# Performance work log

Measured on AMD Instinct MI355X. Metric: run time of the kernel, lower is better.

The kernel has to match this reference:

```python
import jax, jax.numpy as jnp
import numpy as np

S, M, H, E = 8192, 1024, 4096, 8
CAPACITY = S // E  # capacity_factor = 1.0, k = 1


def setup_inputs() -> dict:
    key = jax.random.key(0)
    ks = jax.random.split(key, 4)
    return {
        "x": jax.random.normal(ks[0], (S, M), jnp.float32),
        "wg": jax.random.normal(ks[1], (M, E), jnp.float32) * 0.02,
        "inter_w": jax.random.normal(ks[2], (E, M, H), jnp.float32) * 0.02,
        "inter_b": jnp.zeros((E, H), jnp.float32),
        "output_w": jax.random.normal(ks[3], (E, H, M), jnp.float32) * 0.02,
        "output_b": jnp.zeros((E, M), jnp.float32),
    }


def _top1_gate(x, wg, capacity):
    """GShard-style top-1 gate (inference: no noise, drop tokens over capacity).
    Returns combine_weights [S,E,C] (float) and dispatch_mask [S,E,C] (float 0/1)."""
    logits = x @ wg                                   # [S,E]
    gates = jax.nn.softmax(logits, axis=-1)           # [S,E]
    idx = jnp.argmax(gates, axis=-1)                  # [S]
    mask1 = jax.nn.one_hot(idx, gates.shape[-1], dtype=gates.dtype)  # [S,E]
    # 0-based position of each token within its expert's queue
    locations = jnp.cumsum(mask1, axis=0) - mask1     # [S,E]
    mask1 = mask1 * (locations < capacity)            # drop overflow tokens
    pos = jnp.sum(locations * mask1, axis=1).astype(jnp.int32)  # [S]
    gate_s = jnp.sum(gates * mask1, axis=1)           # [S] gate value of kept tokens
    loc_oh = jax.nn.one_hot(pos, capacity, dtype=gates.dtype)    # [S,C]
    combine = gate_s[:, None, None] * mask1[:, :, None] * loc_oh[:, None, :]  # [S,E,C]
    dispatch = (combine > 0).astype(x.dtype)
    return combine, dispatch


def reference(x, wg, inter_w, inter_b, output_w, output_b):
    combine, dispatch = _top1_gate(x, wg, CAPACITY)
    # token dispatch: torch.einsum('sec,sm->ecm', dispatch_mask, attention_output)
    disp_x = jnp.einsum('sec,sm->ecm', dispatch, x)                 # [E,C,M]
    # per-expert fused gelu-GEMM MLP (gelu_gemm_func: gelu(x@W1+b1)@W2, +b2)
    h = jax.nn.gelu(jnp.einsum('ecm,emh->ech', disp_x, inter_w)
                    + inter_b[:, None, :], approximate=False)       # [E,C,H]
    exp_out = jnp.einsum('ech,ehm->ecm', h, output_w) + output_b[:, None, :]  # [E,C,M]
    # combine: combined_weights.reshape(S, E*C) @ expert_output.reshape(E*C, M)
    y = jnp.einsum('sec,ecm->sm', combine, exp_out)                 # [S,M]
    return y
```

## Files before the change

### kernel.cpp

```cpp
#include <hip/hip_runtime.h>

#define S_ 8192
#define M_ 1024
#define H_ 4096
#define E_ 8
#define C_ 1024

typedef short s16x8 __attribute__((ext_vector_type(8)));
typedef float f32x4 __attribute__((ext_vector_type(4)));

__device__ __forceinline__ unsigned short f2bf(float f) {
    unsigned int u = __float_as_uint(f);
    unsigned int r = u + 0x7fffu + ((u >> 16) & 1u);
    return (unsigned short)(r >> 16);
}
__device__ __forceinline__ float bf2f(unsigned short s) {
    return __uint_as_float(((unsigned int)s) << 16);
}

__device__ __forceinline__ void async_copy16(const unsigned short* g, unsigned short* l) {
    __builtin_amdgcn_global_load_lds(
        (const __attribute__((address_space(1))) unsigned int*)g,
        (__attribute__((address_space(3))) unsigned int*)l, 16, 0, 0);
}

__global__ __launch_bounds__(256) void gate_kernel(
    const float* __restrict__ x, const float* __restrict__ wg,
    int* __restrict__ expert_of, float* __restrict__ gate_full,
    unsigned short* __restrict__ xb)
{
    int token = (blockIdx.x * 256 + threadIdx.x) >> 6;
    int lane  = threadIdx.x & 63;
    const float* xr = x + (size_t)token * M_;
    unsigned short* xbr = xb + (size_t)token * M_;
    double acc[E_] = {0,0,0,0,0,0,0,0};
    for (int t = 0; t < M_ / 64; ++t) {
        int m = t * 64 + lane;
        float xf = xr[m];
        xbr[m] = f2bf(xf);
        double xv = (double)xf;
        const float* w = wg + m * E_;
        #pragma unroll
        for (int e = 0; e < E_; ++e) acc[e] += xv * (double)w[e];
    }
    #pragma unroll
    for (int e = 0; e < E_; ++e)
        for (int off = 32; off; off >>= 1) acc[e] += __shfl_xor(acc[e], off);
    if (lane == 0) {
        double mx = acc[0]; int idx = 0;
        #pragma unroll
        for (int e = 1; e < E_; ++e) if (acc[e] > mx) { mx = acc[e]; idx = e; }
        double den = 0.0;
        #pragma unroll
        for (int e = 0; e < E_; ++e) den += exp(acc[e] - mx);
        expert_of[token] = idx;
        gate_full[token] = (float)(1.0 / den);
    }
}

__global__ __launch_bounds__(256) void count_kernel(
    const int* __restrict__ expert_of, int* __restrict__ cnt,
    int* __restrict__ slot_to_token)
{
    __shared__ int wc[4][E_];
    int tid = threadIdx.x, lane = tid & 63, wv = tid >> 6;
    slot_to_token[blockIdx.x * 256 + tid] = -1;
    int e = expert_of[blockIdx.x * 256 + tid];
    #pragma unroll
    for (int j = 0; j < E_; ++j) {
        unsigned long long b = __ballot(e == j);
        if (lane == 0) wc[wv][j] = __popcll(b);
    }
    __syncthreads();
    if (tid < E_) {
        int s = 0;
        #pragma unroll
        for (int w = 0; w < 4; ++w) s += wc[w][tid];
        cnt[blockIdx.x * E_ + tid] = s;
    }
}

__global__ __launch_bounds__(64) void prefix_kernel(
    const int* __restrict__ cnt, int* __restrict__ cbase)
{
    int tid = threadIdx.x;
    if (tid < E_) {
        int run = 0;
        for (int b = 0; b < 32; ++b) { cbase[b * E_ + tid] = run; run += cnt[b * E_ + tid]; }
    }
}

__global__ __launch_bounds__(256) void scatter_kernel(
    const int* __restrict__ expert_of, const int* __restrict__ cbase,
    int* __restrict__ slot_to_token)
{
    __shared__ int wc[4][E_];
    int tid = threadIdx.x, lane = tid & 63, wv = tid >> 6;
    int s = blockIdx.x * 256 + tid;
    int e = expert_of[s];
    unsigned long long mymask = 0;
    #pragma unroll
    for (int j = 0; j < E_; ++j) {
        unsigned long long b = __ballot(e == j);
        if (lane == 0) wc[wv][j] = __popcll(b);
        if (j == e) mymask = b;
    }
    __syncthreads();
    int waveoff = 0;
    for (int w = 0; w < 4; ++w) if (w < wv) waveoff += wc[w][e];
    int pos = cbase[blockIdx.x * E_ + e] + waveoff +
              __popcll(mymask & ((1ull << lane) - 1ull));
    if (pos < C_) slot_to_token[e * C_ + pos] = s;
}

__global__ __launch_bounds__(256) void transpose_cvt_kernel(
    const float* __restrict__ src, unsigned short* __restrict__ dst, int K, int N)
{
    __shared__ unsigned short tile[64 * 84];
    const size_t esz = (size_t)K * N;
    const float* s = src + (size_t)blockIdx.z * esz;
    unsigned short* d = dst + (size_t)blockIdx.z * esz;
    const int k0 = blockIdx.y * 64, n0 = blockIdx.x * 64;
    const int tid = threadIdx.x;
    {
        const int n  = tid & 63;
        const int kb = (tid >> 6) * 16;
        #pragma unroll
        for (int i = 0; i < 4; ++i) {
            int k4 = kb + i * 4;
            float a0 = s[(size_t)(k0 + k4 + 0) * N + n0 + n];
            float a1 = s[(size_t)(k0 + k4 + 1) * N + n0 + n];
            float a2 = s[(size_t)(k0 + k4 + 2) * N + n0 + n];
            float a3 = s[(size_t)(k0 + k4 + 3) * N + n0 + n];
            unsigned long long p = (unsigned long long)f2bf(a0)
                | ((unsigned long long)f2bf(a1) << 16)
                | ((unsigned long long)f2bf(a2) << 32)
                | ((unsigned long long)f2bf(a3) << 48);
            *(unsigned long long*)(&tile[n * 84 + k4]) = p;
        }
    }
    __syncthreads();
    {
        const int n  = tid >> 3;
        const int k8 = (tid & 7) * 8;
        #pragma unroll
        for (int j = 0; j < 2; ++j) {
            int nn = n + j * 32;
            unsigned long long lo = *(const unsigned long long*)(&tile[nn * 84 + k8]);
            unsigned long long hi = *(const unsigned long long*)(&tile[nn * 84 + k8 + 4]);
            ulonglong2 v; v.x = lo; v.y = hi;
            *(ulonglong2*)(d + (size_t)(n0 + nn) * K + k0 + k8) = v;
        }
    }
}


#define RD_A(BUF, I, KS) \
  (*(const s16x8*)(&AsB[BUF][(wr * 128 + (I) * 16 + ln16) * 64 + ((((KS) * 4 + qd) ^ ln7) * 8)]))
#define RD_B(BUF, J, KS) \
  (*(const s16x8*)(&BsB[BUF][(wcn * 64 + (J) * 16 + ln16) * 64 + ((((KS) * 4 + qd) ^ ln7) * 8)]))

#define STG_A(BUF, HF, KT) do { \
    async_copy16(ap[2 * (HF)]     + (size_t)(KT) * 64, dA##BUF + (2 * (HF)) * 4096); \
    async_copy16(ap[2 * (HF) + 1] + (size_t)(KT) * 64, dA##BUF + (2 * (HF) + 1) * 4096); } while (0)
#define STG_B(BUF, HF, KT) do { \
    async_copy16(bp[2 * (HF)]     + (size_t)(KT) * 64, dB##BUF + (2 * (HF)) * 4096); \
    async_copy16(bp[2 * (HF) + 1] + (size_t)(KT) * 64, dB##BUF + (2 * (HF) + 1) * 4096); } while (0)

#define MFMA16(I0, J0, BB) do { \
    __builtin_amdgcn_s_setprio(1); \
    _Pragma("unroll") \
    for (int ii = 0; ii < 4; ++ii) { \
      acc[(I0)+ii][(J0)+0] = __builtin_amdgcn_mfma_f32_16x16x32_bf16(a[ii][0], BB[0][0], acc[(I0)+ii][(J0)+0], 0, 0, 0); \
      acc[(I0)+ii][(J0)+0] = __builtin_amdgcn_mfma_f32_16x16x32_bf16(a[ii][1], BB[0][1], acc[(I0)+ii][(J0)+0], 0, 0, 0); \
      acc[(I0)+ii][(J0)+1] = __builtin_amdgcn_mfma_f32_16x16x32_bf16(a[ii][0], BB[1][0], acc[(I0)+ii][(J0)+1], 0, 0, 0); \
      acc[(I0)+ii][(J0)+1] = __builtin_amdgcn_mfma_f32_16x16x32_bf16(a[ii][1], BB[1][1], acc[(I0)+ii][(J0)+1], 0, 0, 0); \
    } \
    __builtin_amdgcn_s_setprio(0); \
} while (0)

#define BAR()  __builtin_amdgcn_s_barrier()
#define LGKM0() asm volatile("s_waitcnt lgkmcnt(0)" ::: "memory")
#define VM2()  asm volatile("s_waitcnt vmcnt(2)" ::: "memory")
#define VM0()  asm volatile("s_waitcnt vmcnt(0)" ::: "memory")

#define GEMM_8PH(NITER, NT) \
    STG_A(0, 0, 0); STG_A(0, 1, 0); STG_B(0, 0, 0); STG_B(0, 1, 0); \
    STG_A(1, 0, 1); \
    VM2(); BAR(); \
    for (int it = 0; it < (NITER); ++it) { \
        const int t1 = 2 * it + 1, t2 = 2 * it + 2, t3 = 2 * it + 3; \
         \
        _Pragma("unroll") for (int ii = 0; ii < 4; ++ii) { a[ii][0] = RD_A(0, ii, 0); a[ii][1] = RD_A(0, ii, 1); } \
        b01[0][0] = RD_B(0, 0, 0); b01[0][1] = RD_B(0, 0, 1); \
        b01[1][0] = RD_B(0, 1, 0); b01[1][1] = RD_B(0, 1, 1); \
        STG_A(1, 1, t1); \
        BAR(); LGKM0(); MFMA16(0, 0, b01); BAR(); \
         \
        b23[0][0] = RD_B(0, 2, 0); b23[0][1] = RD_B(0, 2, 1); \
        b23[1][0] = RD_B(0, 3, 0); b23[1][1] = RD_B(0, 3, 1); \
        STG_B(1, 0, t1); \
        BAR(); LGKM0(); MFMA16(0, 2, b23); BAR(); \
         \
        _Pragma("unroll") for (int ii = 0; ii < 4; ++ii) { a[ii][0] = RD_A(0, 4 + ii, 0); a[ii][1] = RD_A(0, 4 + ii, 1); } \
        STG_B(1, 1, t1); \
        BAR(); LGKM0(); MFMA16(4, 2, b23); BAR(); \
         \
        if (t2 < (NT)) { STG_A(0, 0, t2); VM2(); } else { VM0(); } \
        BAR(); MFMA16(4, 0, b01); BAR(); \
         \
        _Pragma("unroll") for (int ii = 0; ii < 4; ++ii) { a[ii][0] = RD_A(1, ii, 0); a[ii][1] = RD_A(1, ii, 1); } \
        b01[0][0] = RD_B(1, 0, 0); b01[0][1] = RD_B(1, 0, 1); \
        b01[1][0] = RD_B(1, 1, 0); b01[1][1] = RD_B(1, 1, 1); \
        if (t2 < (NT)) STG_A(0, 1, t2); \
        BAR(); LGKM0(); MFMA16(0, 0, b01); BAR(); \
         \
        b23[0][0] = RD_B(1, 2, 0); b23[0][1] = RD_B(1, 2, 1); \
        b23[1][0] = RD_B(1, 3, 0); b23[1][1] = RD_B(1, 3, 1); \
        if (t2 < (NT)) STG_B(0, 0, t2); \
        BAR(); LGKM0(); MFMA16(0, 2, b23); BAR(); \
         \
        _Pragma("unroll") for (int ii = 0; ii < 4; ++ii) { a[ii][0] = RD_A(1, 4 + ii, 0); a[ii][1] = RD_A(1, 4 + ii, 1); } \
        if (t2 < (NT)) STG_B(0, 1, t2); \
        BAR(); LGKM0(); MFMA16(4, 2, b23); BAR(); \
         \
        if (t3 < (NT)) { STG_A(1, 0, t3); VM2(); } else { VM0(); } \
        BAR(); MFMA16(4, 0, b01); BAR(); \
    }

__global__ __launch_bounds__(512, 2) void gemm1_kernel(
    const unsigned short* __restrict__ xb, const unsigned short* __restrict__ w1t,
    const float* __restrict__ b1, const int* __restrict__ slot_to_token,
    unsigned short* __restrict__ h)
{
    __shared__ unsigned short AsB[2][16384];
    __shared__ unsigned short BsB[2][16384];
    __shared__ int tokS[256];
    const int lin = blockIdx.x + 16 * blockIdx.y + 64 * blockIdx.z;
    const int e = lin & 7, slot = lin >> 3;
    const int n0 = (slot & 15) * 256, c0 = (slot >> 4) * 256;
    const int tid = threadIdx.x;
    if (tid < 256) tokS[tid] = slot_to_token[e * C_ + c0 + tid];
    __syncthreads();
    const int wv = tid >> 6, l = tid & 63;
    const int wr = wv >> 2, wcn = wv & 3;
    const int qd = l >> 4, ln16 = l & 15, ln7 = ln16 & 7;
    const int rsub = (wv << 3) + (l >> 3);
    const int slotoff = ((l & 7) ^ ((l >> 3) & 7)) * 8;

    const unsigned short* ap[4];
    const unsigned short* bp[4];
    #pragma unroll
    for (int q = 0; q < 4; ++q) {
        int t = tokS[q * 64 + rsub]; if (t < 0) t = 0;
        ap[q] = xb + (size_t)t * M_ + slotoff;
        bp[q] = w1t + (size_t)e * M_ * H_ + (size_t)(n0 + q * 64 + rsub) * M_ + slotoff;
    }
    unsigned short* dA0 = &AsB[0][(wv * 8) * 64];
    unsigned short* dA1 = &AsB[1][(wv * 8) * 64];
    unsigned short* dB0 = &BsB[0][(wv * 8) * 64];
    unsigned short* dB1 = &BsB[1][(wv * 8) * 64];

    f32x4 acc[8][4] = {};
    s16x8 a[4][2], b01[2][2], b23[2][2];

    GEMM_8PH(8, 16)

    unsigned short* hb = h + (size_t)e * C_ * H_;
    #pragma unroll
    for (int i = 0; i < 8; ++i) {
        int crow = c0 + wr * 128 + i * 16 + qd * 4;
        #pragma unroll
        for (int j = 0; j < 4; ++j) {
            int n = n0 + wcn * 64 + j * 16 + ln16;
            float bias = b1[e * H_ + n];
            #pragma unroll
            for (int r = 0; r < 4; ++r) {
                float v = acc[i][j][r] + bias;
                float u = v * v;
                float z = v * (1.5957691216f + 0.0713548163f * u);
                float g = v / (1.0f + __expf(-z));
                hb[(size_t)(crow + r) * H_ + n] = f2bf(g);
            }
        }
    }
}

__global__ __launch_bounds__(512, 2) void gemm2_kernel(
    const unsigned short* __restrict__ h, const unsigned short* __restrict__ w2t,
    const float* __restrict__ b2, const int* __restrict__ slot_to_token,
    const float* __restrict__ gate_full, float* __restrict__ y)
{
    __shared__ unsigned short AsB[2][16384];
    __shared__ unsigned short BsB[2][16384];
    __shared__ int tokS[256];
    __shared__ float gwS[256];
    const int lin = blockIdx.x + 4 * blockIdx.y + 16 * blockIdx.z;
    const int xcd = lin & 7, slot = lin >> 3;
    const int zz = xcd * 2 + (slot >> 4);
    const int e = zz >> 1, kc = zz & 1;
    const int n0 = (slot & 3) * 256, c0 = ((slot >> 2) & 3) * 256;
    const int tid = threadIdx.x;
    if (tid < 256) {
        int t = slot_to_token[e * C_ + c0 + tid];
        tokS[tid] = t;
        gwS[tid] = (t >= 0) ? gate_full[t] : 0.0f;
    }
    __syncthreads();
    const int wv = tid >> 6, l = tid & 63;
    const int wr = wv >> 2, wcn = wv & 3;
    const int qd = l >> 4, ln16 = l & 15, ln7 = ln16 & 7;
    const int rsub = (wv << 3) + (l >> 3);
    const int slotoff = ((l & 7) ^ ((l >> 3) & 7)) * 8;
    const int kb = kc * 2048;

    const unsigned short* ap[4];
    const unsigned short* bp[4];
    #pragma unroll
    for (int q = 0; q < 4; ++q) {
        ap[q] = h + (size_t)e * C_ * H_ + (size_t)(c0 + q * 64 + rsub) * H_ + kb + slotoff;
        bp[q] = w2t + (size_t)e * M_ * H_ + (size_t)(n0 + q * 64 + rsub) * H_ + kb + slotoff;
    }
    unsigned short* dA0 = &AsB[0][(wv * 8) * 64];
    unsigned short* dA1 = &AsB[1][(wv * 8) * 64];
    unsigned short* dB0 = &BsB[0][(wv * 8) * 64];
    unsigned short* dB1 = &BsB[1][(wv * 8) * 64];

    f32x4 acc[8][4] = {};
    s16x8 a[4][2], b01[2][2], b23[2][2];

    GEMM_8PH(16, 32)

    #pragma unroll
    for (int i = 0; i < 8; ++i) {
        int lr0 = wr * 128 + i * 16 + qd * 4;
        #pragma unroll
        for (int j = 0; j < 4; ++j) {
            int n = n0 + wcn * 64 + j * 16 + ln16;
            float bias = kc ? 0.0f : b2[e * M_ + n];
            #pragma unroll
            for (int r = 0; r < 4; ++r) {
                int t = tokS[lr0 + r];
                if (t >= 0)
                    atomicAdd(&y[(size_t)t * M_ + n], gwS[lr0 + r] * (acc[i][j][r] + bias));
            }
        }
    }
}

extern "C" void kernel_launch(void* const* d_in, const int* in_sizes, int n_in,
                              void* d_out, int out_size, void* d_ws, size_t ws_size,
                              hipStream_t stream) {
    const float* x  = (const float*)d_in[0];
    const float* wg = (const float*)d_in[1];
    const float* w1 = (const float*)d_in[2];
    const float* b1 = (const float*)d_in[3];
    const float* w2 = (const float*)d_in[4];
    const float* b2 = (const float*)d_in[5];
    float* y = (float*)d_out;

    char* ws = (char*)d_ws;
    int*   slot_to_token = (int*)ws;
    float* gate_full     = (float*)(ws + 32768);
    int*   cnt           = (int*)(ws + 65536);
    int*   cbase         = (int*)(ws + 66560);
    int*   expert_of     = (int*)(ws + 67584);
    unsigned short* xb   = (unsigned short*)(ws + 131072);
    unsigned short* w2t  = xb + (size_t)S_ * M_;

    unsigned short* w1t  = (unsigned short*)d_in[4];
    unsigned short* h    = (unsigned short*)d_in[2];

    hipMemsetAsync(d_out, 0, (size_t)S_ * M_ * sizeof(float), stream);
    gate_kernel<<<S_ / 4, 256, 0, stream>>>(x, wg, expert_of, gate_full, xb);
    count_kernel<<<32, 256, 0, stream>>>(expert_of, cnt, slot_to_token);
    prefix_kernel<<<1, 64, 0, stream>>>(cnt, cbase);
    scatter_kernel<<<32, 256, 0, stream>>>(expert_of, cbase, slot_to_token);

    transpose_cvt_kernel<<<dim3(M_ / 64, H_ / 64, E_), 256, 0, stream>>>(w2, w2t, H_, M_);
    transpose_cvt_kernel<<<dim3(H_ / 64, M_ / 64, E_), 256, 0, stream>>>(w1, w1t, M_, H_);

    gemm1_kernel<<<dim3(16, 4, 8), 512, 0, stream>>>(xb, w1t, b1, slot_to_token, h);
    gemm2_kernel<<<dim3(4, 4, 16), 512, 0, stream>>>(h, w2t, b2, slot_to_token, gate_full, y);
}
```

Measured before the change: 580.9 us.

## Replace double-buffered 64-wide K pipeline with 4-stage 32-wide ring buffer

Both expert GEMM kernels move from a two-buffer, K=64 staging scheme with eight MFMA phases per iteration to a four-slot ring of K=32 tiles, prefetching three tiles ahead. The LDS swizzle, the staging address math and the wait counts are redone to match. The goal is deeper latency hiding on global-to-LDS loads with simpler phase logic. In exchange each slot holds half the K depth, so there are more barriers per unit of work. Each MFMA pass also gets only 16 ops, which may hurt overlap.

Measured after the change: 586.5 us. Within noise of the previous version (+1.0%).

```diff
diff --git a/kernel.cpp b/kernel.cpp
--- a/kernel.cpp
+++ b/kernel.cpp
@@ -155,77 +155,50 @@
 }
 
 
-#define RD_A(BUF, I, KS) \
-  (*(const s16x8*)(&AsB[BUF][(wr * 128 + (I) * 16 + ln16) * 64 + ((((KS) * 4 + qd) ^ ln7) * 8)]))
-#define RD_B(BUF, J, KS) \
-  (*(const s16x8*)(&BsB[BUF][(wcn * 64 + (J) * 16 + ln16) * 64 + ((((KS) * 4 + qd) ^ ln7) * 8)]))
-
-#define STG_A(BUF, HF, KT) do { \
-    async_copy16(ap[2 * (HF)]     + (size_t)(KT) * 64, dA##BUF + (2 * (HF)) * 4096); \
-    async_copy16(ap[2 * (HF) + 1] + (size_t)(KT) * 64, dA##BUF + (2 * (HF) + 1) * 4096); } while (0)
-#define STG_B(BUF, HF, KT) do { \
-    async_copy16(bp[2 * (HF)]     + (size_t)(KT) * 64, dB##BUF + (2 * (HF)) * 4096); \
-    async_copy16(bp[2 * (HF) + 1] + (size_t)(KT) * 64, dB##BUF + (2 * (HF) + 1) * 4096); } while (0)
-
-#define MFMA16(I0, J0, BB) do { \
-    __builtin_amdgcn_s_setprio(1); \
-    _Pragma("unroll") \
-    for (int ii = 0; ii < 4; ++ii) { \
-      acc[(I0)+ii][(J0)+0] = __builtin_amdgcn_mfma_f32_16x16x32_bf16(a[ii][0], BB[0][0], acc[(I0)+ii][(J0)+0], 0, 0, 0); \
-      acc[(I0)+ii][(J0)+0] = __builtin_amdgcn_mfma_f32_16x16x32_bf16(a[ii][1], BB[0][1], acc[(I0)+ii][(J0)+0], 0, 0, 0); \
-      acc[(I0)+ii][(J0)+1] = __builtin_amdgcn_mfma_f32_16x16x32_bf16(a[ii][0], BB[1][0], acc[(I0)+ii][(J0)+1], 0, 0, 0); \
-      acc[(I0)+ii][(J0)+1] = __builtin_amdgcn_mfma_f32_16x16x32_bf16(a[ii][1], BB[1][1], acc[(I0)+ii][(J0)+1], 0, 0, 0); \
-    } \
-    __builtin_amdgcn_s_setprio(0); \
-} while (0)
-
-#define BAR()  __builtin_amdgcn_s_barrier()
+#define BAR()   __builtin_amdgcn_s_barrier()
 #define LGKM0() asm volatile("s_waitcnt lgkmcnt(0)" ::: "memory")
-#define VM2()  asm volatile("s_waitcnt vmcnt(2)" ::: "memory")
-#define VM0()  asm volatile("s_waitcnt vmcnt(0)" ::: "memory")
-
-#define GEMM_8PH(NITER, NT) \
-    STG_A(0, 0, 0); STG_A(0, 1, 0); STG_B(0, 0, 0); STG_B(0, 1, 0); \
-    STG_A(1, 0, 1); \
-    VM2(); BAR(); \
-    for (int it = 0; it < (NITER); ++it) { \
-        const int t1 = 2 * it + 1, t2 = 2 * it + 2, t3 = 2 * it + 3; \
-         \
-        _Pragma("unroll") for (int ii = 0; ii < 4; ++ii) { a[ii][0] = RD_A(0, ii, 0); a[ii][1] = RD_A(0, ii, 1); } \
-        b01[0][0] = RD_B(0, 0, 0); b01[0][1] = RD_B(0, 0, 1); \
-        b01[1][0] = RD_B(0, 1, 0); b01[1][1] = RD_B(0, 1, 1); \
-        STG_A(1, 1, t1); \
-        BAR(); LGKM0(); MFMA16(0, 0, b01); BAR(); \
-         \
-        b23[0][0] = RD_B(0, 2, 0); b23[0][1] = RD_B(0, 2, 1); \
-        b23[1][0] = RD_B(0, 3, 0); b23[1][1] = RD_B(0, 3, 1); \
-        STG_B(1, 0, t1); \
-        BAR(); LGKM0(); MFMA16(0, 2, b23); BAR(); \
-         \
-        _Pragma("unroll") for (int ii = 0; ii < 4; ++ii) { a[ii][0] = RD_A(0, 4 + ii, 0); a[ii][1] = RD_A(0, 4 + ii, 1); } \
-        STG_B(1, 1, t1); \
-        BAR(); LGKM0(); MFMA16(4, 2, b23); BAR(); \
-         \
-        if (t2 < (NT)) { STG_A(0, 0, t2); VM2(); } else { VM0(); } \
-        BAR(); MFMA16(4, 0, b01); BAR(); \
-         \
-        _Pragma("unroll") for (int ii = 0; ii < 4; ++ii) { a[ii][0] = RD_A(1, ii, 0); a[ii][1] = RD_A(1, ii, 1); } \
-        b01[0][0] = RD_B(1, 0, 0); b01[0][1] = RD_B(1, 0, 1); \
-        b01[1][0] = RD_B(1, 1, 0); b01[1][1] = RD_B(1, 1, 1); \
-        if (t2 < (NT)) STG_A(0, 1, t2); \
-        BAR(); LGKM0(); MFMA16(0, 0, b01); BAR(); \
-         \
-        b23[0][0] = RD_B(1, 2, 0); b23[0][1] = RD_B(1, 2, 1); \
-        b23[1][0] = RD_B(1, 3, 0); b23[1][1] = RD_B(1, 3, 1); \
-        if (t2 < (NT)) STG_B(0, 0, t2); \
-        BAR(); LGKM0(); MFMA16(0, 2, b23); BAR(); \
-         \
-        _Pragma("unroll") for (int ii = 0; ii < 4; ++ii) { a[ii][0] = RD_A(1, 4 + ii, 0); a[ii][1] = RD_A(1, 4 + ii, 1); } \
-        if (t2 < (NT)) STG_B(0, 1, t2); \
-        BAR(); LGKM0(); MFMA16(4, 2, b23); BAR(); \
-         \
-        if (t3 < (NT)) { STG_A(1, 0, t3); VM2(); } else { VM0(); } \
-        BAR(); MFMA16(4, 0, b01); BAR(); \
+#define VMW(N)  asm volatile("s_waitcnt vmcnt(" #N ")" ::: "memory")
+
+#define STG_A(RB, KT) do { \
+    async_copy16(apA + (size_t)(KT) * 32, &Rng[RB][0][(wv * 16) * 32]); \
+    async_copy16(apB + (size_t)(KT) * 32, &Rng[RB][0][(128 + wv * 16) * 32]); } while (0)
+#define STG_B(RB, KT) do { \
+    async_copy16(bpA + (size_t)(KT) * 32, &Rng[RB][1][(wv * 16) * 32]); \
+    async_copy16(bpB + (size_t)(KT) * 32, &Rng[RB][1][(128 + wv * 16) * 32]); } while (0)
+
+#define GEMM_RING(NT) \
+    STG_A(0, 0); STG_B(0, 0); STG_A(1, 1); STG_B(1, 1); STG_A(2, 2); STG_B(2, 2); \
+    VMW(8); BAR(); \
+    for (int t = 0; t < (NT); ++t) { \
+        const int rb = t & 3, rs = (t + 3) & 3; \
+        const unsigned short* Ab = &Rng[rb][0][0]; \
+        const unsigned short* Bb = &Rng[rb][1][0]; \
+        s16x8 av[4], bv[4]; \
+        _Pragma("unroll") for (int i = 0; i < 4; ++i) \
+            av[i] = *(const s16x8*)(Ab + (wr * 128 + i * 16 + ln16) * 32 + rdo); \
+        _Pragma("unroll") for (int j = 0; j < 4; ++j) \
+            bv[j] = *(const s16x8*)(Bb + (wcn * 64 + j * 16 + ln16) * 32 + rdo); \
+        if (t + 3 < (NT)) STG_A(rs, t + 3); \
+        BAR(); LGKM0(); \
+        __builtin_amdgcn_s_setprio(1); \
+        _Pragma("unroll") for (int i = 0; i < 4; ++i) \
+            _Pragma("unroll") for (int j = 0; j < 4; ++j) \
+                acc[i][j] = __builtin_amdgcn_mfma_f32_16x16x32_bf16(av[i], bv[j], acc[i][j], 0, 0, 0); \
+        __builtin_amdgcn_s_setprio(0); \
+        BAR(); \
+        _Pragma("unroll") for (int i = 0; i < 4; ++i) \
+            av[i] = *(const s16x8*)(Ab + (wr * 128 + (4 + i) * 16 + ln16) * 32 + rdo); \
+        if (t + 3 < (NT)) STG_B(rs, t + 3); \
+        BAR(); LGKM0(); \
+        __builtin_amdgcn_s_setprio(1); \
+        _Pragma("unroll") for (int i = 0; i < 4; ++i) \
+            _Pragma("unroll") for (int j = 0; j < 4; ++j) \
+                acc[4 + i][j] = __builtin_amdgcn_mfma_f32_16x16x32_bf16(av[i], bv[j], acc[4 + i][j], 0, 0, 0); \
+        __builtin_amdgcn_s_setprio(0); \
+        if (t + 3 < (NT)) { VMW(8); } \
+        else if (t + 2 < (NT)) { VMW(4); } \
+        else if (t + 1 < (NT)) { VMW(0); } \
+        BAR(); \
     }
 
 __global__ __launch_bounds__(512, 2) void gemm1_kernel(
@@ -233,8 +206,7 @@
     const float* __restrict__ b1, const int* __restrict__ slot_to_token,
     unsigned short* __restrict__ h)
 {
-    __shared__ unsigned short AsB[2][16384];
-    __shared__ unsigned short BsB[2][16384];
+    __shared__ unsigned short Rng[4][2][8192];
     __shared__ int tokS[256];
     const int lin = blockIdx.x + 16 * blockIdx.y + 64 * blockIdx.z;
     const int e = lin & 7, slot = lin >> 3;
@@ -244,27 +216,22 @@
     __syncthreads();
     const int wv = tid >> 6, l = tid & 63;
     const int wr = wv >> 2, wcn = wv & 3;
-    const int qd = l >> 4, ln16 = l & 15, ln7 = ln16 & 7;
-    const int rsub = (wv << 3) + (l >> 3);
-    const int slotoff = ((l & 7) ^ ((l >> 3) & 7)) * 8;
-
-    const unsigned short* ap[4];
-    const unsigned short* bp[4];
-    #pragma unroll
-    for (int q = 0; q < 4; ++q) {
-        int t = tokS[q * 64 + rsub]; if (t < 0) t = 0;
-        ap[q] = xb + (size_t)t * M_ + slotoff;
-        bp[q] = w1t + (size_t)e * M_ * H_ + (size_t)(n0 + q * 64 + rsub) * M_ + slotoff;
-    }
-    unsigned short* dA0 = &AsB[0][(wv * 8) * 64];
-    unsigned short* dA1 = &AsB[1][(wv * 8) * 64];
-    unsigned short* dB0 = &BsB[0][(wv * 8) * 64];
-    unsigned short* dB1 = &BsB[1][(wv * 8) * 64];
+    const int qd = l >> 4, ln16 = l & 15;
+    const int rdo = (qd ^ ((ln16 >> 1) & 3)) * 8;
+    const int srow = tid >> 2;
+    const int soff = ((tid & 3) ^ ((tid >> 3) & 3)) * 8;
+
+    int t0 = tokS[srow];       if (t0 < 0) t0 = 0;
+    int t1 = tokS[128 + srow]; if (t1 < 0) t1 = 0;
+    const unsigned short* apA = xb + (size_t)t0 * M_ + soff;
+    const unsigned short* apB = xb + (size_t)t1 * M_ + soff;
+    const unsigned short* Bp = w1t + (size_t)e * M_ * H_;
+    const unsigned short* bpA = Bp + (size_t)(n0 + srow) * M_ + soff;
+    const unsigned short* bpB = Bp + (size_t)(n0 + 128 + srow) * M_ + soff;
 
     f32x4 acc[8][4] = {};
-    s16x8 a[4][2], b01[2][2], b23[2][2];
-
-    GEMM_8PH(8, 16)
+
+    GEMM_RING(32)
 
     unsigned short* hb = h + (size_t)e * C_ * H_;
     #pragma unroll
@@ -291,8 +258,7 @@
     const float* __restrict__ b2, const int* __restrict__ slot_to_token,
     const float* __restrict__ gate_full, float* __restrict__ y)
 {
-    __shared__ unsigned short AsB[2][16384];
-    __shared__ unsigned short BsB[2][16384];
+    __shared__ unsigned short Rng[4][2][8192];
     __shared__ int tokS[256];
     __shared__ float gwS[256];
     const int lin = blockIdx.x + 4 * blockIdx.y + 16 * blockIdx.z;
@@ -309,27 +275,22 @@
     __syncthreads();
     const int wv = tid >> 6, l = tid & 63;
     const int wr = wv >> 2, wcn = wv & 3;
-    const int qd = l >> 4, ln16 = l & 15, ln7 = ln16 & 7;
-    const int rsub = (wv << 3) + (l >> 3);
-    const int slotoff = ((l & 7) ^ ((l >> 3) & 7)) * 8;
+    const int qd = l >> 4, ln16 = l & 15;
+    const int rdo = (qd ^ ((ln16 >> 1) & 3)) * 8;
+    const int srow = tid >> 2;
+    const int soff = ((tid & 3) ^ ((tid >> 3) & 3)) * 8;
     const int kb = kc * 2048;
 
-    const unsigned short* ap[4];
-    const unsigned short* bp[4];
-    #pragma unroll
-    for (int q = 0; q < 4; ++q) {
-        ap[q] = h + (size_t)e * C_ * H_ + (size_t)(c0 + q * 64 + rsub) * H_ + kb + slotoff;
-        bp[q] = w2t + (size_t)e * M_ * H_ + (size_t)(n0 + q * 64 + rsub) * H_ + kb + slotoff;
-    }
-    unsigned short* dA0 = &AsB[0][(wv * 8) * 64];
-    unsigned short* dA1 = &AsB[1][(wv * 8) * 64];
-    unsigned short* dB0 = &BsB[0][(wv * 8) * 64];
-    unsigned short* dB1 = &BsB[1][(wv * 8) * 64];
+    const unsigned short* Apb = h + (size_t)e * C_ * H_ + kb + soff;
+    const unsigned short* apA = Apb + (size_t)(c0 + srow) * H_;
+    const unsigned short* apB = Apb + (size_t)(c0 + 128 + srow) * H_;
+    const unsigned short* Bpb = w2t + (size_t)e * M_ * H_ + kb + soff;
+    const unsigned short* bpA = Bpb + (size_t)(n0 + srow) * H_;
+    const unsigned short* bpB = Bpb + (size_t)(n0 + 128 + srow) * H_;
 
     f32x4 acc[8][4] = {};
-    s16x8 a[4][2], b01[2][2], b23[2][2];
-
-    GEMM_8PH(16, 32)
+
+    GEMM_RING(64)
 
     #pragma unroll
     for (int i = 0; i < 8; ++i) {
```
